# Kernel optimization log

Measured on AMD Instinct MI355X. Metric: run time of the kernel, lower is better.

## Reference

```python
import jax, jax.numpy as jnp
import numpy as np

# Sparse MinkUNet-style backbone sizes
N0, N1, N2, N3 = 100000, 50000, 25000, 12500  # voxels per level (batch-concatenated)
K, KD = 27, 8        # 3x3x3 kernel offsets, stride-2 child offsets
B, S = 8, 1024       # batch, seed_num
C0, C1, C2, C3 = 32, 64, 128, 256
COUT = 512


def _w(k, shape, fan_in):
    return jax.random.normal(k, shape, dtype=jnp.float32) / np.sqrt(fan_in)


def setup_inputs() -> dict:
    key = jax.random.key(0)
    ks = jax.random.split(key, 32)
    inp = {}
    inp["feats"] = jax.random.normal(ks[0], (N0, 3), dtype=jnp.float32)
    # neighbor maps (kernel-offset gather indices, as built by a voxel hash map)
    inp["nbr0"] = jax.random.randint(ks[1], (N0, K), 0, N0, dtype=jnp.int32)
    inp["nbr1"] = jax.random.randint(ks[2], (N1, K), 0, N1, dtype=jnp.int32)
    inp["nbr2"] = jax.random.randint(ks[3], (N2, K), 0, N2, dtype=jnp.int32)
    inp["nbr3"] = jax.random.randint(ks[4], (N3, K), 0, N3, dtype=jnp.int32)
    # stride-2 downsample maps (coarse voxel -> fine children)
    inp["down1"] = jax.random.randint(ks[5], (N1, KD), 0, N0, dtype=jnp.int32)
    inp["down2"] = jax.random.randint(ks[6], (N2, KD), 0, N1, dtype=jnp.int32)
    inp["down3"] = jax.random.randint(ks[7], (N3, KD), 0, N2, dtype=jnp.int32)
    # nearest-parent upsample maps (fine voxel -> coarse parent)
    inp["up2"] = jax.random.randint(ks[8], (N2,), 0, N3, dtype=jnp.int32)
    inp["up1"] = jax.random.randint(ks[9], (N1,), 0, N2, dtype=jnp.int32)
    inp["up0"] = jax.random.randint(ks[10], (N0,), 0, N1, dtype=jnp.int32)
    # nearest-voxel devoxelize index for each FPS seed point
    inp["seed_idx"] = jax.random.randint(ks[11], (B, S), 0, N0, dtype=jnp.int32)
    # conv kernels [K, Cin, Cout] and 1x1 (linear) decoder weights
    inp["W_stem"] = _w(ks[12], (K, 3, C0), K * 3)
    inp["W_b0"] = _w(ks[13], (K, C0, C0), K * C0)
    inp["W_d1"] = _w(ks[14], (KD, C0, C1), KD * C0)
    inp["W_b1"] = _w(ks[15], (K, C1, C1), K * C1)
    inp["W_d2"] = _w(ks[16], (KD, C1, C2), KD * C1)
    inp["W_b2"] = _w(ks[17], (K, C2, C2), K * C2)
    inp["W_d3"] = _w(ks[18], (KD, C2, C3), KD * C2)
    inp["W_b3"] = _w(ks[19], (K, C3, C3), K * C3)
    inp["W_u2"] = _w(ks[20], (C3 + C2, 256), C3 + C2)
    inp["W_u1"] = _w(ks[21], (256 + C1, 128), 256 + C1)
    inp["W_u0"] = _w(ks[22], (128 + C0, 96), 128 + C0)
    inp["W_out"] = _w(ks[23], (96, COUT), 96)
    return inp


def sp_conv(f, nbr, W):
    # gather neighbor features then contract over (kernel offset, in-channel)
    g = f[nbr]                                # [N, K, Cin]
    return jnp.einsum('nkc,kco->no', g, W)    # [N, Cout]


def reference(feats, nbr0, nbr1, nbr2, nbr3, down1, down2, down3,
              up2, up1, up0, seed_idx,
              W_stem, W_b0, W_d1, W_b1, W_d2, W_b2, W_d3, W_b3,
              W_u2, W_u1, W_u0, W_out):
    relu = jax.nn.relu
    # encoder
    x0 = relu(sp_conv(feats, nbr0, W_stem))          # [N0, 32]
    x0 = x0 + relu(sp_conv(x0, nbr0, W_b0))
    x1 = relu(sp_conv(x0, down1, W_d1))              # [N1, 64]
    x1 = x1 + relu(sp_conv(x1, nbr1, W_b1))
    x2 = relu(sp_conv(x1, down2, W_d2))              # [N2, 128]
    x2 = x2 + relu(sp_conv(x2, nbr2, W_b2))
    x3 = relu(sp_conv(x2, down3, W_d3))              # [N3, 256]
    x3 = x3 + relu(sp_conv(x3, nbr3, W_b3))
    # decoder: nearest-parent upsample + skip concat + 1x1 conv
    u2 = relu(jnp.concatenate([x3[up2], x2], axis=-1) @ W_u2)   # [N2, 256]
    u1 = relu(jnp.concatenate([u2[up1], x1], axis=-1) @ W_u1)   # [N1, 128]
    u0 = relu(jnp.concatenate([u1[up0], x0], axis=-1) @ W_u0)   # [N0, 96]
    out_vox = u0 @ W_out                                        # [N0, 512]
    seed_feats = out_vox[seed_idx]                              # [B, S, 512]
    return jnp.transpose(seed_feats, (0, 2, 1))                 # [B, 512, S]
```

## Files before the change

### kernel.cpp

```cpp
#include <hip/hip_runtime.h>

typedef unsigned short u16;
typedef unsigned int u32;
typedef __bf16 bf16x8 __attribute__((ext_vector_type(8)));
typedef float f32x4 __attribute__((ext_vector_type(4)));
typedef u16 u16x4 __attribute__((ext_vector_type(4)));

#define NV0 100000
#define NV1 50000
#define NV2 25000
#define NV3 12500

enum : long {
  OFF_WB0  = 0,
  OFF_WD1  = 27648,
  OFF_WB1  = 44032,
  OFF_WD2  = 154624,
  OFF_WB2  = 220160,
  OFF_WD3  = 662528,
  OFF_WB3  = 924672,
  OFF_WU2  = 2694144,
  OFF_WU1  = 2792448,
  OFF_WU0  = 2833408,
  OFF_WOUT = 2848768,
  OFF_TA   = 2897920,
  OFF_X0   = OFF_TA  + 3200000,
  OFF_X1   = OFF_X0  + 3200000,
  OFF_X2   = OFF_X1  + 3200000,
  OFF_X3   = OFF_X2  + 3200000,
  OFF_U2   = OFF_X3  + 3200000,
  OFF_U1   = OFF_U2  + 6400000,
  OFF_U0S  = OFF_U1  + 6400000,
  OFF_END  = OFF_U0S + 786432,
};

__device__ __forceinline__ float b2f(u16 u) {
  union { u32 i; float f; } x; x.i = ((u32)u) << 16; return x.f;
}
__device__ __forceinline__ u16 f2b(float f) {
  union { float f; u32 i; } x; x.f = f;
  u32 r = (x.i + 0x7FFFu + ((x.i >> 16) & 1u)) >> 16;
  return (u16)r;
}
__device__ __forceinline__ void gload16(const u16* g, const u16* l) {
  __builtin_amdgcn_global_load_lds(
      (const __attribute__((address_space(1))) void*)g,
      (__attribute__((address_space(3))) void*)(u16*)l, 16, 0, 0);
}
__device__ __forceinline__ void store_out(u16* p, float v)  { *p = f2b(v); }
__device__ __forceinline__ void store_out(float* p, float v) { *p = v; }
constexpr int ilog2c(int x) { return x <= 1 ? 0 : 1 + ilog2c(x / 2); }

struct PD { const float* src; u16* dst; int KK, CIN, COUT; };
struct PrepArgs { PD d[11]; };

__global__ __launch_bounds__(256) void prep_k(PrepArgs pa) {
  const PD d = pa.d[blockIdx.y];
  const int cc = d.CIN * d.COUT;
  const int total = d.KK * cc;
  for (int e = blockIdx.x * 256 + threadIdx.x; e < total; e += gridDim.x * 256) {
    int k = e / cc;
    int r = e - k * cc;
    int c = r / d.COUT;
    int o = r - c * d.COUT;
    d.dst[(k * d.COUT + o) * d.CIN + c] = f2b(d.src[e]);
  }
}

__global__ __launch_bounds__(256) void stem_k(const float* __restrict__ feats,
                                              const int* __restrict__ nbr0,
                                              const float* __restrict__ wstem,
                                              u16* __restrict__ out) {
  __shared__ float Wl[27 * 3 * 32];
  const int tid = threadIdx.x;
  for (int i = tid; i < 2592; i += 256) Wl[i] = wstem[i];
  __syncthreads();
  const int n = blockIdx.x * 8 + (tid >> 5);
  const int o = tid & 31;
  if (n >= NV0) return;
  float acc = 0.f;
  const int* nb = nbr0 + n * 27;
  #pragma unroll
  for (int k = 0; k < 27; k++) {
    const int iv = nb[k];
    const float* f = feats + iv * 3;
    acc = fmaf(f[0], Wl[(k * 3 + 0) * 32 + o], acc);
    acc = fmaf(f[1], Wl[(k * 3 + 1) * 32 + o], acc);
    acc = fmaf(f[2], Wl[(k * 3 + 2) * 32 + o], acc);
  }
  out[n * 32 + o] = f2b(fmaxf(acc, 0.f));
}

template <int BM, int BN, int WM, int WN, int COUTF, int KCT, int BK, int MODE,
          int CIN, int KK, int CA, int KSPL, int NCB, int SWZ,
          bool RES, bool DORELU, typename OT>
__global__ __launch_bounds__(256, 4) void gemm_k(
    const u16* __restrict__ src0, const u16* __restrict__ src1,
    const int* __restrict__ idx0, const int* __restrict__ idx1,
    const u16* __restrict__ wt, const u16* __restrict__ base,
    OT* __restrict__ out, int N) {
  constexpr int NWM = BM / WM, NWN = BN / WN;
  static_assert(NWM * NWN == 4, "4 waves");
  constexpr int MI = WM / 16, NI = WN / 16;
  constexpr int CB = KCT - CA;
  constexpr int SLOTS = BK / 8;
  constexpr int SM = SLOTS - 1;
  constexpr int LSL = ilog2c(SLOTS);
  constexpr int RPC = 64 / SLOTS;
  constexpr int LRPC = ilog2c(RPC);
  constexpr int ACH = (BM * BK) / 512;
  constexpr int BCH = (BN * BK) / 512;
  constexpr int NIT = KCT / BK / KSPL;
  constexpr int LOGC = ilog2c(CIN);
  constexpr int ATRIPS = ACH / 4;
  constexpr int CTRIPS = (ACH + BCH + 3) / 4;
  constexpr int NIDX = (MODE == 0) ? BM * KK : (MODE == 3 ? 1 : 2 * BM);
  static_assert(ACH % 4 == 0, "A chunks divisible by wave count");
  static_assert(KCT % (BK * KSPL) == 0, "K mult of BK*KSPL");
  static_assert((MODE != 1 && MODE != 2) || (CA % BK == 0), "concat boundary aligned");
  static_assert(KSPL == 1 || MODE == 0, "split only for sparse conv");

  __shared__ u16 As[2][BM * BK];
  __shared__ u16 Bs[2][BN * BK];
  __shared__ int Is[NIDX];
  const int tid = threadIdx.x;
  const int w = tid >> 6, lane = tid & 63;
  const int quad = lane >> 4, l16 = lane & 15;
  const int wm = w % NWM, wn = w / NWM;

  int row0, col0, kbz;
  if constexpr (SWZ) {
    const int NBR = (N + BM - 1) / BM;
    const int R = NBR * KSPL;
    const int wg = blockIdx.x;
    const int xc = wg & 7, j = wg >> 3;
    const int cb = j % NCB, t = j / NCB;
    const int rt = t * 8 + xc;
    if (rt >= R) return;
    row0 = (rt / KSPL) * BM;
    kbz  = rt % KSPL;
    col0 = cb * BN;
  } else {
    row0 = blockIdx.x * BM;
    col0 = blockIdx.y * BN;
    kbz  = blockIdx.z;
  }
  const int Nm1 = N - 1;
  const int srow = lane >> LSL;
  const int g    = (lane & SM) ^ (srow & SM);
  const int cl   = g * 8;

  if constexpr (MODE == 0) {
    for (int e = tid; e < BM * KK; e += 256) {
      const int r = e / KK, k = e - r * KK;
      int n = row0 + r; n = (n > Nm1) ? Nm1 : n;
      Is[e] = idx0[(long)n * KK + k] * CIN;
    }
  } else if constexpr (MODE == 1) {
    for (int e = tid; e < BM; e += 256) {
      int n = row0 + e; n = (n > Nm1) ? Nm1 : n;
      Is[e] = idx0[n] * CA;
      Is[BM + e] = n * CB;
    }
  } else if constexpr (MODE == 2) {
    for (int e = tid; e < BM; e += 256) {
      int n = row0 + e; n = (n > Nm1) ? Nm1 : n;
      const int s = idx0[n];
      Is[e] = idx1[s] * CA;
      Is[BM + e] = s * CB;
    }
  }
  if constexpr (MODE != 3) __syncthreads();

  int pre[CTRIPS];
  #pragma unroll
  for (int t = 0; t < CTRIPS; t++) {
    const int c = w + 4 * t;
    if (t < ATRIPS) {
      const int r = (c << LRPC) + srow;
      if constexpr (MODE == 0) {
        pre[t] = (r * KK + (cl >> LOGC)) * 4;
      } else if constexpr (MODE == 3) {
        int n = row0 + r; n = (n > Nm1) ? Nm1 : n;
        pre[t] = n * KCT + cl;
      } else {
        pre[t] = r * 4;
      }
    } else if (c < ACH + BCH) {
      const int o = col0 + ((c - ACH) << LRPC) + srow;
      if constexpr (MODE == 0)
        pre[t] = (cl >> LOGC) * (COUTF * CIN) + o * CIN + (cl & (CIN - 1));
      else
        pre[t] = o * KCT + cl;
    }
  }
  const int claneA = (MODE == 0) ? (cl & (CIN - 1)) : cl;

  f32x4 acc[MI][NI];
  #pragma unroll
  for (int i = 0; i < MI; i++)
    #pragma unroll
    for (int j = 0; j < NI; j++) acc[i][j] = {0.f, 0.f, 0.f, 0.f};

  auto stage = [&](int buf, int kc0) {
    int kadd = 0, cadd = 0, kcc = 0;
    const u16* sA = src0;
    if constexpr (MODE == 0) {
      kadd = (kc0 >> LOGC) * 4;
      cadd = kc0 & (CIN - 1);
      kcc  = (kc0 >> LOGC) * (COUTF * CIN) + cadd;
    } else if constexpr (MODE == 1 || MODE == 2) {
      if (kc0 >= CA) { kadd = BM * 4; cadd = kc0 - CA; sA = src1; }
      else           { cadd = kc0; }
    }
    #pragma unroll
    for (int t = 0; t < CTRIPS; t++) {
      const int c = w + 4 * t;
      if constexpr (CTRIPS * 4 > ACH + BCH) { if (c >= ACH + BCH) continue; }
      if (t < ATRIPS) {
        int off;
        if constexpr (MODE == 3) off = pre[t] + kc0;
        else off = *(const int*)((const char*)Is + (pre[t] + kadd)) + cadd + claneA;
        gload16(sA + off, &As[buf][c * 512]);
      } else {
        int off;
        if constexpr (MODE == 0) off = pre[t] + kcc;
        else                     off = pre[t] + kc0;
        gload16(wt + off, &Bs[buf][(c - ACH) * 512]);
      }
    }
  };

  const int kb = (KSPL > 1) ? kbz * (KCT / KSPL) : 0;
  stage(0, kb);
  #pragma unroll 1
  for (int it = 0; it < NIT; it++) {
    __syncthreads();
    if (it + 1 < NIT) stage((it + 1) & 1, kb + (it + 1) * BK);
    const int buf = it & 1;
    #pragma unroll
    for (int kk = 0; kk < BK / 32; kk++) {
      bf16x8 af[MI], bfr[NI];
      #pragma unroll
      for (int i = 0; i < MI; i++) {
        const int row = wm * WM + i * 16 + l16;
        const int slot = row * SLOTS + (((kk << 2) + quad) ^ (row & SM));
        af[i] = *(const bf16x8*)&As[buf][slot * 8];
      }
      #pragma unroll
      for (int j = 0; j < NI; j++) {
        const int row = wn * WN + j * 16 + l16;
        const int slot = row * SLOTS + (((kk << 2) + quad) ^ (row & SM));
        bfr[j] = *(const bf16x8*)&Bs[buf][slot * 8];
      }
      #pragma unroll
      for (int i = 0; i < MI; i++)
        #pragma unroll
        for (int j = 0; j < NI; j++)
          acc[i][j] = __builtin_amdgcn_mfma_f32_16x16x32_bf16(af[i], bfr[j], acc[i][j], 0, 0, 0);
    }
  }

  OT* op = out;
  if constexpr (KSPL > 1) op += (long)kbz * ((long)N * COUTF);
  #pragma unroll
  for (int i = 0; i < MI; i++) {
    #pragma unroll
    for (int j = 0; j < NI; j++) {
      const int col = col0 + wn * WN + j * 16 + l16;
      #pragma unroll
      for (int r = 0; r < 4; r++) {
        const int n = row0 + wm * WM + i * 16 + quad * 4 + r;
        if (n < N) {
          float v = acc[i][j][r];
          if constexpr (RES)         v = b2f(base[(long)n * COUTF + col]) + fmaxf(v, 0.f);
          else if constexpr (DORELU) v = fmaxf(v, 0.f);
          store_out(&op[(long)n * COUTF + col], v);
        }
      }
    }
  }
}

__global__ __launch_bounds__(256) void fix_k(const float* __restrict__ p0,
                                             const float* __restrict__ p1,
                                             const u16* __restrict__ base,
                                             u16* __restrict__ out) {
  const long i = ((long)blockIdx.x * 256 + threadIdx.x) * 4;
  const f32x4 a = *(const f32x4*)(p0 + i);
  const f32x4 b = *(const f32x4*)(p1 + i);
  const u16x4 bs = *(const u16x4*)(base + i);
  u16x4 r;
  #pragma unroll
  for (int j = 0; j < 4; j++) r[j] = f2b(b2f(bs[j]) + fmaxf(a[j] + b[j], 0.f));
  *(u16x4*)(out + i) = r;
}

__global__ __launch_bounds__(256) void tout_k(const float* __restrict__ tmp,
                                              float* __restrict__ outp) {
  __shared__ float tl[64][65];
  const int tid = threadIdx.x;
  const int r0 = blockIdx.x * 64, o0 = blockIdx.y * 64;
  {
    const int rl = tid >> 2, oc = (tid & 3) * 16;
    const float* src = &tmp[(r0 + rl) * 512 + o0 + oc];
    #pragma unroll
    for (int j = 0; j < 16; j++) tl[rl][oc + j] = src[j];
  }
  __syncthreads();
  {
    const int ol = tid >> 2, sc = (tid & 3) * 16;
    const int b = r0 >> 10, s0 = r0 & 1023;
    float* dst = &outp[((long)b * 512 + (o0 + ol)) * 1024 + s0 + sc];
    #pragma unroll
    for (int j = 0; j < 16; j++) dst[j] = tl[sc + j][ol];
  }
}

static inline int swz_grid(int N, int BM, int KSPL, int NCB) {
  const int nbr = (N + BM - 1) / BM;
  const int rp = ((nbr * KSPL + 7) / 8) * 8;
  return rp * NCB;
}

extern "C" void kernel_launch(void* const* d_in, const int* in_sizes, int n_in,
                              void* d_out, int out_size, void* d_ws, size_t ws_size,
                              hipStream_t stream) {
  const float* feats = (const float*)d_in[0];
  const int* nbr0  = (const int*)d_in[1];
  const int* nbr1  = (const int*)d_in[2];
  const int* nbr2  = (const int*)d_in[3];
  const int* nbr3  = (const int*)d_in[4];
  const int* down1 = (const int*)d_in[5];
  const int* down2 = (const int*)d_in[6];
  const int* down3 = (const int*)d_in[7];
  const int* up2   = (const int*)d_in[8];
  const int* up1   = (const int*)d_in[9];
  const int* up0   = (const int*)d_in[10];
  const int* seed  = (const int*)d_in[11];
  u16* ws = (u16*)d_ws;

  PrepArgs pa;
  pa.d[0]  = {(const float*)d_in[13], ws + OFF_WB0,  27, 32, 32};
  pa.d[1]  = {(const float*)d_in[14], ws + OFF_WD1,  8,  32, 64};
  pa.d[2]  = {(const float*)d_in[15], ws + OFF_WB1,  27, 64, 64};
  pa.d[3]  = {(const float*)d_in[16], ws + OFF_WD2,  8,  64, 128};
  pa.d[4]  = {(const float*)d_in[17], ws + OFF_WB2,  27, 128, 128};
  pa.d[5]  = {(const float*)d_in[18], ws + OFF_WD3,  8,  128, 256};
  pa.d[6]  = {(const float*)d_in[19], ws + OFF_WB3,  27, 256, 256};
  pa.d[7]  = {(const float*)d_in[20], ws + OFF_WU2,  1,  384, 256};
  pa.d[8]  = {(const float*)d_in[21], ws + OFF_WU1,  1,  320, 128};
  pa.d[9]  = {(const float*)d_in[22], ws + OFF_WU0,  1,  160, 96};
  pa.d[10] = {(const float*)d_in[23], ws + OFF_WOUT, 1,  96,  512};
  prep_k<<<dim3(128, 11), 256, 0, stream>>>(pa);

  u16* ta  = ws + OFF_TA;
  u16* x0  = ws + OFF_X0;
  u16* x1  = ws + OFF_X1;
  u16* x2  = ws + OFF_X2;
  u16* x3  = ws + OFF_X3;
  u16* u2b = ws + OFF_U2;
  u16* u1b = ws + OFF_U1;
  u16* u0s = ws + OFF_U0S;
  float* tmp  = (float*)(ws + OFF_TA);
  float* part = (float*)(ws + OFF_U2);

  stem_k<<<12500, 256, 0, stream>>>(feats, nbr0, (const float*)d_in[12], ta);

  gemm_k<128, 32, 32, 32, 32, 864, 32, 0, 32, 27, 0, 1, 1, 1, true, true, u16>
      <<<swz_grid(NV0, 128, 1, 1), 256, 0, stream>>>(ta, nullptr, nbr0, nullptr, ws + OFF_WB0, ta, x0, NV0);
  gemm_k<64, 64, 32, 32, 64, 256, 64, 0, 32, 8, 0, 1, 1, 1, false, true, u16>
      <<<swz_grid(NV1, 64, 1, 1), 256, 0, stream>>>(x0, nullptr, down1, nullptr, ws + OFF_WD1, nullptr, ta, NV1);
  gemm_k<64, 64, 32, 32, 64, 1728, 64, 0, 64, 27, 0, 1, 1, 1, true, true, u16>
      <<<swz_grid(NV1, 64, 1, 1), 256, 0, stream>>>(ta, nullptr, nbr1, nullptr, ws + OFF_WB1, ta, x1, NV1);
  gemm_k<64, 64, 32, 32, 128, 512, 64, 0, 64, 8, 0, 1, 2, 1, false, true, u16>
      <<<swz_grid(NV2, 64, 1, 2), 256, 0, stream>>>(x1, nullptr, down2, nullptr, ws + OFF_WD2, nullptr, ta, NV2);
  gemm_k<64, 64, 32, 32, 128, 3456, 64, 0, 128, 27, 0, 2, 2, 1, false, false, float>
      <<<swz_grid(NV2, 64, 2, 2), 256, 0, stream>>>(ta, nullptr, nbr2, nullptr, ws + OFF_WB2, nullptr, part, NV2);
  fix_k<<<dim3(3125), 256, 0, stream>>>(part, part + 3200000, ta, x2);
  gemm_k<64, 64, 32, 32, 256, 1024, 64, 0, 128, 8, 0, 1, 4, 1, false, true, u16>
      <<<swz_grid(NV3, 64, 1, 4), 256, 0, stream>>>(x2, nullptr, down3, nullptr, ws + OFF_WD3, nullptr, ta, NV3);
  gemm_k<64, 64, 32, 32, 256, 6912, 64, 0, 256, 27, 0, 2, 4, 1, false, false, float>
      <<<swz_grid(NV3, 64, 2, 4), 256, 0, stream>>>(ta, nullptr, nbr3, nullptr, ws + OFF_WB3, nullptr, part, NV3);
  fix_k<<<dim3(3125), 256, 0, stream>>>(part, part + 3200000, ta, x3);
  gemm_k<64, 64, 32, 32, 256, 384, 64, 1, 32, 1, 256, 1, 4, 1, false, true, u16>
      <<<swz_grid(NV2, 64, 1, 4), 256, 0, stream>>>(x3, x2, up2, nullptr, ws + OFF_WU2, nullptr, u2b, NV2);
  gemm_k<64, 64, 32, 32, 128, 320, 64, 1, 32, 1, 256, 1, 2, 1, false, true, u16>
      <<<swz_grid(NV1, 64, 1, 2), 256, 0, stream>>>(u2b, x1, up1, nullptr, ws + OFF_WU1, nullptr, u1b, NV1);
  gemm_k<64, 96, 32, 48, 96, 160, 32, 2, 32, 1, 128, 1, 1, 0, false, true, u16>
      <<<dim3(128, 1), 256, 0, stream>>>(u1b, x0, seed, up0, ws + OFF_WU0, nullptr, u0s, 8192);
  gemm_k<64, 64, 32, 32, 512, 96, 32, 3, 32, 1, 0, 1, 1, 0, false, false, float>
      <<<dim3(128, 8), 256, 0, stream>>>(u0s, nullptr, nullptr, nullptr, ws + OFF_WOUT, nullptr, tmp, 8192);
  tout_k<<<dim3(128, 8), 256, 0, stream>>>(tmp, (float*)d_out);
}
```

Baseline: 490.8 us.

## Split-K the level-0 and level-1 residual convs and fix the LDS swizzle for narrow tiles

The b0 and b1 submanifold convs now use three-way split-K. Each split writes fp32 partials into spare x1/x2 buffers, and an extended fix kernel sums the three partials, applies relu and adds the residual. This gives these large convs more parallel work. The LDS XOR swizzle now shifts the row before masking when BK is small (BK=32), which should remove bank conflicts in that configuration. In exchange the change adds extra fp32 partial traffic and one more kernel launch per layer. The new fix kernel also reads the residual base with scalar loads instead of a vector load.

```diff
diff --git a/kernel.cpp b/kernel.cpp
--- a/kernel.cpp
+++ b/kernel.cpp
@@ -106,6 +106,7 @@
   constexpr int SLOTS = BK / 8;
   constexpr int SM = SLOTS - 1;
   constexpr int LSL = ilog2c(SLOTS);
+  constexpr int RSH = (LSL >= 3) ? 0 : (3 - LSL);
   constexpr int RPC = 64 / SLOTS;
   constexpr int LRPC = ilog2c(RPC);
   constexpr int ACH = (BM * BK) / 512;
@@ -147,7 +148,7 @@
   }
   const int Nm1 = N - 1;
   const int srow = lane >> LSL;
-  const int g    = (lane & SM) ^ (srow & SM);
+  const int g    = (lane & SM) ^ ((srow >> RSH) & SM);
   const int cl   = g * 8;
 
   if constexpr (MODE == 0) {
@@ -244,13 +245,13 @@
       #pragma unroll
       for (int i = 0; i < MI; i++) {
         const int row = wm * WM + i * 16 + l16;
-        const int slot = row * SLOTS + (((kk << 2) + quad) ^ (row & SM));
+        const int slot = row * SLOTS + (((kk << 2) + quad) ^ ((row >> RSH) & SM));
         af[i] = *(const bf16x8*)&As[buf][slot * 8];
       }
       #pragma unroll
       for (int j = 0; j < NI; j++) {
         const int row = wn * WN + j * 16 + l16;
-        const int slot = row * SLOTS + (((kk << 2) + quad) ^ (row & SM));
+        const int slot = row * SLOTS + (((kk << 2) + quad) ^ ((row >> RSH) & SM));
         bfr[j] = *(const bf16x8*)&Bs[buf][slot * 8];
       }
       #pragma unroll
@@ -282,17 +283,24 @@
   }
 }
 
+template <int NP, bool HB>
 __global__ __launch_bounds__(256) void fix_k(const float* __restrict__ p0,
                                              const float* __restrict__ p1,
+                                             const float* __restrict__ p2,
                                              const u16* __restrict__ base,
                                              u16* __restrict__ out) {
   const long i = ((long)blockIdx.x * 256 + threadIdx.x) * 4;
   const f32x4 a = *(const f32x4*)(p0 + i);
   const f32x4 b = *(const f32x4*)(p1 + i);
-  const u16x4 bs = *(const u16x4*)(base + i);
+  f32x4 c = {0.f, 0.f, 0.f, 0.f};
+  if constexpr (NP == 3) c = *(const f32x4*)(p2 + i);
   u16x4 r;
   #pragma unroll
-  for (int j = 0; j < 4; j++) r[j] = f2b(b2f(bs[j]) + fmaxf(a[j] + b[j], 0.f));
+  for (int j = 0; j < 4; j++) {
+    float v = fmaxf(a[j] + b[j] + c[j], 0.f);
+    if constexpr (HB) v += b2f(base[i + j]);
+    r[j] = f2b(v);
+  }
   *(u16x4*)(out + i) = r;
 }
 
@@ -364,25 +372,29 @@
   u16* u0s = ws + OFF_U0S;
   float* tmp  = (float*)(ws + OFF_TA);
   float* part = (float*)(ws + OFF_U2);
+  float* pb0  = (float*)(ws + OFF_X1);
+  float* pb1  = (float*)(ws + OFF_X2);
 
   stem_k<<<12500, 256, 0, stream>>>(feats, nbr0, (const float*)d_in[12], ta);
 
-  gemm_k<128, 32, 32, 32, 32, 864, 32, 0, 32, 27, 0, 1, 1, 1, true, true, u16>
-      <<<swz_grid(NV0, 128, 1, 1), 256, 0, stream>>>(ta, nullptr, nbr0, nullptr, ws + OFF_WB0, ta, x0, NV0);
+  gemm_k<128, 32, 32, 32, 32, 864, 32, 0, 32, 27, 0, 3, 1, 1, false, false, float>
+      <<<swz_grid(NV0, 128, 3, 1), 256, 0, stream>>>(ta, nullptr, nbr0, nullptr, ws + OFF_WB0, nullptr, pb0, NV0);
+  fix_k<3, true><<<dim3(3125), 256, 0, stream>>>(pb0, pb0 + 3200000, pb0 + 6400000, ta, x0);
   gemm_k<64, 64, 32, 32, 64, 256, 64, 0, 32, 8, 0, 1, 1, 1, false, true, u16>
       <<<swz_grid(NV1, 64, 1, 1), 256, 0, stream>>>(x0, nullptr, down1, nullptr, ws + OFF_WD1, nullptr, ta, NV1);
-  gemm_k<64, 64, 32, 32, 64, 1728, 64, 0, 64, 27, 0, 1, 1, 1, true, true, u16>
-      <<<swz_grid(NV1, 64, 1, 1), 256, 0, stream>>>(ta, nullptr, nbr1, nullptr, ws + OFF_WB1, ta, x1, NV1);
+  gemm_k<64, 64, 32, 32, 64, 1728, 64, 0, 64, 27, 0, 3, 1, 1, false, false, float>
+      <<<swz_grid(NV1, 64, 3, 1), 256, 0, stream>>>(ta, nullptr, nbr1, nullptr, ws + OFF_WB1, nullptr, pb1, NV1);
+  fix_k<3, true><<<dim3(3125), 256, 0, stream>>>(pb1, pb1 + 3200000, pb1 + 6400000, ta, x1);
   gemm_k<64, 64, 32, 32, 128, 512, 64, 0, 64, 8, 0, 1, 2, 1, false, true, u16>
       <<<swz_grid(NV2, 64, 1, 2), 256, 0, stream>>>(x1, nullptr, down2, nullptr, ws + OFF_WD2, nullptr, ta, NV2);
   gemm_k<64, 64, 32, 32, 128, 3456, 64, 0, 128, 27, 0, 2, 2, 1, false, false, float>
       <<<swz_grid(NV2, 64, 2, 2), 256, 0, stream>>>(ta, nullptr, nbr2, nullptr, ws + OFF_WB2, nullptr, part, NV2);
-  fix_k<<<dim3(3125), 256, 0, stream>>>(part, part + 3200000, ta, x2);
+  fix_k<2, true><<<dim3(3125), 256, 0, stream>>>(part, part + 3200000, nullptr, ta, x2);
   gemm_k<64, 64, 32, 32, 256, 1024, 64, 0, 128, 8, 0, 1, 4, 1, false, true, u16>
       <<<swz_grid(NV3, 64, 1, 4), 256, 0, stream>>>(x2, nullptr, down3, nullptr, ws + OFF_WD3, nullptr, ta, NV3);
   gemm_k<64, 64, 32, 32, 256, 6912, 64, 0, 256, 27, 0, 2, 4, 1, false, false, float>
       <<<swz_grid(NV3, 64, 2, 4), 256, 0, stream>>>(ta, nullptr, nbr3, nullptr, ws + OFF_WB3, nullptr, part, NV3);
-  fix_k<<<dim3(3125), 256, 0, stream>>>(part, part + 3200000, ta, x3);
+  fix_k<2, true><<<dim3(3125), 256, 0, stream>>>(part, part + 3200000, nullptr, ta, x3);
   gemm_k<64, 64, 32, 32, 256, 384, 64, 1, 32, 1, 256, 1, 4, 1, false, true, u16>
       <<<swz_grid(NV2, 64, 1, 4), 256, 0, stream>>>(x3, x2, up2, nullptr, ws + OFF_WU2, nullptr, u2b, NV2);
   gemm_k<64, 64, 32, 32, 128, 320, 64, 1, 32, 1, 256, 1, 2, 1, false, true, u16>
```

Result: slower. 517.9 us (+5.5%).

## Load weight fragments directly from global memory instead of staging through LDS

Applied to the files above, without the earlier changes.

Removes the shared-memory B tile. Each wave now loads its bf16 weight MFMA fragments straight from global memory into registers, issued before the next A-tile stage. Warp tiles change to 64x16 so each wave covers all rows and a narrow column slice, and launch bounds rise to 5 blocks per CU because the kernel uses less LDS. The intent is to cut LDS traffic and barrier-bound work for the weights, relying on cache hits for the reused weights. The cost is uncoalesced-ish global loads sitting on the critical path, and a changed A swizzle for narrow BK.

```diff
diff --git a/kernel.cpp b/kernel.cpp
--- a/kernel.cpp
+++ b/kernel.cpp
@@ -94,7 +94,7 @@
 template <int BM, int BN, int WM, int WN, int COUTF, int KCT, int BK, int MODE,
           int CIN, int KK, int CA, int KSPL, int NCB, int SWZ,
           bool RES, bool DORELU, typename OT>
-__global__ __launch_bounds__(256, 4) void gemm_k(
+__global__ __launch_bounds__(256, 5) void gemm_k(
     const u16* __restrict__ src0, const u16* __restrict__ src1,
     const int* __restrict__ idx0, const int* __restrict__ idx1,
     const u16* __restrict__ wt, const u16* __restrict__ base,
@@ -106,22 +106,22 @@
   constexpr int SLOTS = BK / 8;
   constexpr int SM = SLOTS - 1;
   constexpr int LSL = ilog2c(SLOTS);
+  constexpr int RSH = (LSL >= 3) ? 0 : (3 - LSL);
   constexpr int RPC = 64 / SLOTS;
   constexpr int LRPC = ilog2c(RPC);
   constexpr int ACH = (BM * BK) / 512;
-  constexpr int BCH = (BN * BK) / 512;
   constexpr int NIT = KCT / BK / KSPL;
   constexpr int LOGC = ilog2c(CIN);
   constexpr int ATRIPS = ACH / 4;
-  constexpr int CTRIPS = (ACH + BCH + 3) / 4;
+  constexpr int KKI = BK / 32;
   constexpr int NIDX = (MODE == 0) ? BM * KK : (MODE == 3 ? 1 : 2 * BM);
   static_assert(ACH % 4 == 0, "A chunks divisible by wave count");
   static_assert(KCT % (BK * KSPL) == 0, "K mult of BK*KSPL");
   static_assert((MODE != 1 && MODE != 2) || (CA % BK == 0), "concat boundary aligned");
   static_assert(KSPL == 1 || MODE == 0, "split only for sparse conv");
+  static_assert(CIN >= 32, "B fragment within one k for a 32-slice");
 
   __shared__ u16 As[2][BM * BK];
-  __shared__ u16 Bs[2][BN * BK];
   __shared__ int Is[NIDX];
   const int tid = threadIdx.x;
   const int w = tid >> 6, lane = tid & 63;
@@ -147,7 +147,7 @@
   }
   const int Nm1 = N - 1;
   const int srow = lane >> LSL;
-  const int g    = (lane & SM) ^ (srow & SM);
+  const int g    = (lane & SM) ^ ((srow >> RSH) & SM);
   const int cl   = g * 8;
 
   if constexpr (MODE == 0) {
@@ -172,30 +172,30 @@
   }
   if constexpr (MODE != 3) __syncthreads();
 
-  int pre[CTRIPS];
-  #pragma unroll
-  for (int t = 0; t < CTRIPS; t++) {
+  int pre[ATRIPS];
+  #pragma unroll
+  for (int t = 0; t < ATRIPS; t++) {
     const int c = w + 4 * t;
-    if (t < ATRIPS) {
-      const int r = (c << LRPC) + srow;
-      if constexpr (MODE == 0) {
-        pre[t] = (r * KK + (cl >> LOGC)) * 4;
-      } else if constexpr (MODE == 3) {
-        int n = row0 + r; n = (n > Nm1) ? Nm1 : n;
-        pre[t] = n * KCT + cl;
-      } else {
-        pre[t] = r * 4;
-      }
-    } else if (c < ACH + BCH) {
-      const int o = col0 + ((c - ACH) << LRPC) + srow;
-      if constexpr (MODE == 0)
-        pre[t] = (cl >> LOGC) * (COUTF * CIN) + o * CIN + (cl & (CIN - 1));
-      else
-        pre[t] = o * KCT + cl;
+    const int r = (c << LRPC) + srow;
+    if constexpr (MODE == 0) {
+      pre[t] = (r * KK + (cl >> LOGC)) * 4;
+    } else if constexpr (MODE == 3) {
+      int n = row0 + r; n = (n > Nm1) ? Nm1 : n;
+      pre[t] = n * KCT + cl;
+    } else {
+      pre[t] = r * 4;
     }
   }
   const int claneA = (MODE == 0) ? (cl & (CIN - 1)) : cl;
 
+  int bo[NI];
+  #pragma unroll
+  for (int j = 0; j < NI; j++) {
+    const int o = col0 + wn * WN + j * 16 + l16;
+    if constexpr (MODE == 0) bo[j] = o * CIN + quad * 8;
+    else                     bo[j] = o * KCT + quad * 8;
+  }
+
   f32x4 acc[MI][NI];
   #pragma unroll
   for (int i = 0; i < MI; i++)
@@ -203,31 +203,22 @@
     for (int j = 0; j < NI; j++) acc[i][j] = {0.f, 0.f, 0.f, 0.f};
 
   auto stage = [&](int buf, int kc0) {
-    int kadd = 0, cadd = 0, kcc = 0;
+    int kadd = 0, cadd = 0;
     const u16* sA = src0;
     if constexpr (MODE == 0) {
       kadd = (kc0 >> LOGC) * 4;
       cadd = kc0 & (CIN - 1);
-      kcc  = (kc0 >> LOGC) * (COUTF * CIN) + cadd;
     } else if constexpr (MODE == 1 || MODE == 2) {
       if (kc0 >= CA) { kadd = BM * 4; cadd = kc0 - CA; sA = src1; }
       else           { cadd = kc0; }
     }
     #pragma unroll
-    for (int t = 0; t < CTRIPS; t++) {
+    for (int t = 0; t < ATRIPS; t++) {
       const int c = w + 4 * t;
-      if constexpr (CTRIPS * 4 > ACH + BCH) { if (c >= ACH + BCH) continue; }
-      if (t < ATRIPS) {
-        int off;
-        if constexpr (MODE == 3) off = pre[t] + kc0;
-        else off = *(const int*)((const char*)Is + (pre[t] + kadd)) + cadd + claneA;
-        gload16(sA + off, &As[buf][c * 512]);
-      } else {
-        int off;
-        if constexpr (MODE == 0) off = pre[t] + kcc;
-        else                     off = pre[t] + kc0;
-        gload16(wt + off, &Bs[buf][(c - ACH) * 512]);
-      }
+      int off;
+      if constexpr (MODE == 3) off = pre[t] + kc0;
+      else off = *(const int*)((const char*)Is + (pre[t] + kadd)) + cadd + claneA;
+      gload16(sA + off, &As[buf][c * 512]);
     }
   };
 
@@ -235,29 +226,35 @@
   stage(0, kb);
   #pragma unroll 1
   for (int it = 0; it < NIT; it++) {
+    const int kc0 = kb + it * BK;
     __syncthreads();
-    if (it + 1 < NIT) stage((it + 1) & 1, kb + (it + 1) * BK);
+    bf16x8 bfr[KKI][NI];
+    #pragma unroll
+    for (int kk = 0; kk < KKI; kk++) {
+      const int kc = kc0 + kk * 32;
+      int ksc;
+      if constexpr (MODE == 0) ksc = (kc >> LOGC) * (COUTF * CIN) + (kc & (CIN - 1));
+      else                     ksc = kc;
+      #pragma unroll
+      for (int j = 0; j < NI; j++)
+        bfr[kk][j] = *(const bf16x8*)(wt + ksc + bo[j]);
+    }
+    if (it + 1 < NIT) stage((it + 1) & 1, kc0 + BK);
     const int buf = it & 1;
     #pragma unroll
-    for (int kk = 0; kk < BK / 32; kk++) {
-      bf16x8 af[MI], bfr[NI];
+    for (int kk = 0; kk < KKI; kk++) {
+      bf16x8 af[MI];
       #pragma unroll
       for (int i = 0; i < MI; i++) {
         const int row = wm * WM + i * 16 + l16;
-        const int slot = row * SLOTS + (((kk << 2) + quad) ^ (row & SM));
+        const int slot = row * SLOTS + (((kk << 2) + quad) ^ ((row >> RSH) & SM));
         af[i] = *(const bf16x8*)&As[buf][slot * 8];
-      }
-      #pragma unroll
-      for (int j = 0; j < NI; j++) {
-        const int row = wn * WN + j * 16 + l16;
-        const int slot = row * SLOTS + (((kk << 2) + quad) ^ (row & SM));
-        bfr[j] = *(const bf16x8*)&Bs[buf][slot * 8];
       }
       #pragma unroll
       for (int i = 0; i < MI; i++)
         #pragma unroll
         for (int j = 0; j < NI; j++)
-          acc[i][j] = __builtin_amdgcn_mfma_f32_16x16x32_bf16(af[i], bfr[j], acc[i][j], 0, 0, 0);
+          acc[i][j] = __builtin_amdgcn_mfma_f32_16x16x32_bf16(af[i], bfr[kk][j], acc[i][j], 0, 0, 0);
     }
   }
 
@@ -369,27 +366,27 @@
 
   gemm_k<128, 32, 32, 32, 32, 864, 32, 0, 32, 27, 0, 1, 1, 1, true, true, u16>
       <<<swz_grid(NV0, 128, 1, 1), 256, 0, stream>>>(ta, nullptr, nbr0, nullptr, ws + OFF_WB0, ta, x0, NV0);
-  gemm_k<64, 64, 32, 32, 64, 256, 64, 0, 32, 8, 0, 1, 1, 1, false, true, u16>
+  gemm_k<64, 64, 64, 16, 64, 256, 64, 0, 32, 8, 0, 1, 1, 1, false, true, u16>
       <<<swz_grid(NV1, 64, 1, 1), 256, 0, stream>>>(x0, nullptr, down1, nullptr, ws + OFF_WD1, nullptr, ta, NV1);
-  gemm_k<64, 64, 32, 32, 64, 1728, 64, 0, 64, 27, 0, 1, 1, 1, true, true, u16>
+  gemm_k<64, 64, 64, 16, 64, 1728, 64, 0, 64, 27, 0, 1, 1, 1, true, true, u16>
       <<<swz_grid(NV1, 64, 1, 1), 256, 0, stream>>>(ta, nullptr, nbr1, nullptr, ws + OFF_WB1, ta, x1, NV1);
-  gemm_k<64, 64, 32, 32, 128, 512, 64, 0, 64, 8, 0, 1, 2, 1, false, true, u16>
+  gemm_k<64, 64, 64, 16, 128, 512, 64, 0, 64, 8, 0, 1, 2, 1, false, true, u16>
       <<<swz_grid(NV2, 64, 1, 2), 256, 0, stream>>>(x1, nullptr, down2, nullptr, ws + OFF_WD2, nullptr, ta, NV2);
-  gemm_k<64, 64, 32, 32, 128, 3456, 64, 0, 128, 27, 0, 2, 2, 1, false, false, float>
+  gemm_k<64, 64, 64, 16, 128, 3456, 64, 0, 128, 27, 0, 2, 2, 1, false, false, float>
       <<<swz_grid(NV2, 64, 2, 2), 256, 0, stream>>>(ta, nullptr, nbr2, nullptr, ws + OFF_WB2, nullptr, part, NV2);
   fix_k<<<dim3(3125), 256, 0, stream>>>(part, part + 3200000, ta, x2);
-  gemm_k<64, 64, 32, 32, 256, 1024, 64, 0, 128, 8, 0, 1, 4, 1, false, true, u16>
+  gemm_k<64, 64, 64, 16, 256, 1024, 64, 0, 128, 8, 0, 1, 4, 1, false, true, u16>
       <<<swz_grid(NV3, 64, 1, 4), 256, 0, stream>>>(x2, nullptr, down3, nullptr, ws + OFF_WD3, nullptr, ta, NV3);
-  gemm_k<64, 64, 32, 32, 256, 6912, 64, 0, 256, 27, 0, 2, 4, 1, false, false, float>
+  gemm_k<64, 64, 64, 16, 256, 6912, 64, 0, 256, 27, 0, 2, 4, 1, false, false, float>
       <<<swz_grid(NV3, 64, 2, 4), 256, 0, stream>>>(ta, nullptr, nbr3, nullptr, ws + OFF_WB3, nullptr, part, NV3);
   fix_k<<<dim3(3125), 256, 0, stream>>>(part, part + 3200000, ta, x3);
-  gemm_k<64, 64, 32, 32, 256, 384, 64, 1, 32, 1, 256, 1, 4, 1, false, true, u16>
+  gemm_k<64, 64, 64, 16, 256, 384, 64, 1, 32, 1, 256, 1, 4, 1, false, true, u16>
       <<<swz_grid(NV2, 64, 1, 4), 256, 0, stream>>>(x3, x2, up2, nullptr, ws + OFF_WU2, nullptr, u2b, NV2);
-  gemm_k<64, 64, 32, 32, 128, 320, 64, 1, 32, 1, 256, 1, 2, 1, false, true, u16>
+  gemm_k<64, 64, 64, 16, 128, 320, 64, 1, 32, 1, 256, 1, 2, 1, false, true, u16>
       <<<swz_grid(NV1, 64, 1, 2), 256, 0, stream>>>(u2b, x1, up1, nullptr, ws + OFF_WU1, nullptr, u1b, NV1);
   gemm_k<64, 96, 32, 48, 96, 160, 32, 2, 32, 1, 128, 1, 1, 0, false, true, u16>
       <<<dim3(128, 1), 256, 0, stream>>>(u1b, x0, seed, up0, ws + OFF_WU0, nullptr, u0s, 8192);
-  gemm_k<64, 64, 32, 32, 512, 96, 32, 3, 32, 1, 0, 1, 1, 0, false, false, float>
+  gemm_k<64, 64, 64, 16, 512, 96, 32, 3, 32, 1, 0, 1, 1, 0, false, false, float>
       <<<dim3(128, 8), 256, 0, stream>>>(u0s, nullptr, nullptr, nullptr, ws + OFF_WOUT, nullptr, tmp, 8192);
   tout_k<<<dim3(128, 8), 256, 0, stream>>>(tmp, (float*)d_out);
 }
```

After: 581.0 us. 1.18x slower.
